# Kernel tuning notes

Measured on AMD Instinct MI355X. Metric: run time of the kernel, lower is better.

## Reference

```python
import jax, jax.numpy as jnp
import numpy as np

N_NODES = 100_000
N_EDGES = 1_600_000
F_DIM = 32


def setup_inputs() -> dict:
    key = jax.random.key(0)
    k1, k2, k3 = jax.random.split(key, 3)
    x = jax.random.normal(k1, (N_NODES, F_DIM), dtype=jnp.float32)
    edge_index = jax.random.randint(k2, (2, N_EDGES), 0, N_NODES, dtype=jnp.int64)
    edge_weight = jax.random.uniform(k3, (N_EDGES,), dtype=jnp.float32)
    w_mp = jnp.array([0.5], dtype=jnp.float32)  # learned scalar parameter
    return {"x": x, "edge_index": edge_index, "edge_weight": edge_weight, "w_mp": w_mp}


def reference(x, edge_index, edge_weight, w_mp):
    # message: ea = w_mp * x[src] * edge_weight  (shape [E, F])
    # aggregate: sum messages into target nodes (aggr='add', source_to_target)
    src = edge_index[0]
    dst = edge_index[1]
    ea = (w_mp * x[src]) * edge_weight[:, None]          # [E, F]
    out = jax.ops.segment_sum(ea, dst, num_segments=x.shape[0])  # [N, F]
    return out
```

## Files before the change

### kernel.cpp

```cpp
#include <hip/hip_runtime.h>


constexpr int N_NODES = 100000;
constexpr int N_EDGES = 1600000;
constexpr int F_DIM   = 32;

constexpr int NPB = 64;
constexpr int NB  = (N_NODES + NPB - 1) / NPB;
constexpr int CAP = 1344;

constexpr int BIN_THREADS = 512;
constexpr int BIN_EPT     = 8;
constexpr int BIN_CHUNK   = BIN_THREADS * BIN_EPT;
constexpr int BIN_BLOCKS  = (N_EDGES + BIN_CHUNK - 1) / BIN_CHUNK;

constexpr int AGG_THREADS = 512;
constexpr int RPT = (CAP + AGG_THREADS - 1) / AGG_THREADS;

constexpr size_t WS_CURSOR  = 0;
constexpr size_t WS_RECORDS = 8192;
constexpr size_t WS_NEEDED  = WS_RECORDS + (size_t)NB * CAP * 8;

__global__ __launch_bounds__(256) void init_cursors(int* __restrict__ gcursor)
{
    int i = blockIdx.x * 256 + threadIdx.x;
    if (i < NB) gcursor[i] = i * CAP;
}

__global__ __launch_bounds__(BIN_THREADS) void bin_edges(
    const int* __restrict__ src, const int* __restrict__ dst,
    const float* __restrict__ ew, const float* __restrict__ w_mp,
    int* __restrict__ gcursor, uint2* __restrict__ records)
{
    __shared__ int lhist[NB];
    __shared__ int lbase[NB];
    for (int i = threadIdx.x; i < NB; i += BIN_THREADS) lhist[i] = 0;
    __syncthreads();

    const float w = w_mp[0];
    const int base_e = blockIdx.x * BIN_CHUNK;
    int   bkt[BIN_EPT];
    uint2 rec[BIN_EPT];

    #pragma unroll
    for (int i = 0; i < BIN_EPT; ++i) {
        int e = base_e + threadIdx.x + i * BIN_THREADS;
        bkt[i] = -1;
        if (e < N_EDGES) {
            int d = dst[e];
            int b = d >> 6;
            bkt[i] = b;
            rec[i].x = __float_as_uint(w * ew[e]);
            rec[i].y = (unsigned)src[e] | ((unsigned)(d & 63) << 24);
            atomicAdd(&lhist[b], 1);
        }
    }
    __syncthreads();

    for (int i = threadIdx.x; i < NB; i += BIN_THREADS) {
        int c = lhist[i];
        lbase[i] = c ? atomicAdd(&gcursor[i], c) : 0;
        lhist[i] = 0;
    }
    __syncthreads();

    #pragma unroll
    for (int i = 0; i < BIN_EPT; ++i) {
        int b = bkt[i];
        if (b >= 0) {
            int pos = lbase[b] + atomicAdd(&lhist[b], 1);
            if (pos < (b + 1) * CAP)
                records[pos] = rec[i];
        }
    }
}

__global__ __launch_bounds__(AGG_THREADS) void sort_gather(
    const int*   __restrict__ gcursor,
    const uint2* __restrict__ records,
    const float* __restrict__ x,
    float*       __restrict__ out)
{
    __shared__ uint2 sorted[CAP];
    __shared__ int   hist[NPB];
    __shared__ int   offs[NPB + 1];
    __shared__ int   cursor[NPB];

    const int b     = blockIdx.x;
    const int t     = threadIdx.x;
    const int rbase = b * CAP;
    const int cnt   = min(gcursor[b] - rbase, CAP);

    if (t < NPB) hist[t] = 0;
    __syncthreads();

    uint2 rec[RPT];
    #pragma unroll
    for (int i = 0; i < RPT; ++i) {
        int j = t + i * AGG_THREADS;
        rec[i].y = 0xFFFFFFFFu;
        if (j < cnt) {
            rec[i] = records[rbase + j];
            atomicAdd(&hist[rec[i].y >> 24], 1);
        }
    }
    __syncthreads();

    if (t < 64) {
        int v   = hist[t];
        int inc = v;
        #pragma unroll
        for (int d = 1; d < 64; d <<= 1) {
            int o = __shfl_up(inc, d, 64);
            if (t >= d) inc += o;
        }
        offs[t + 1] = inc;
        if (t == 0) offs[0] = 0;
        cursor[t] = inc - v;
    }
    __syncthreads();

    #pragma unroll
    for (int i = 0; i < RPT; ++i) {
        if (rec[i].y != 0xFFFFFFFFu) {
            int dl   = rec[i].y >> 24;
            int slot = atomicAdd(&cursor[dl], 1);
            sorted[slot] = rec[i];
        }
    }
    __syncthreads();

    const int node  = t >> 3;
    const int q     = (t & 7) * 4;
    const int gnode = b * NPB + node;
    if (gnode >= N_NODES) return;

    int j  = offs[node];
    int je = offs[node + 1];
    float4 acc = make_float4(0.f, 0.f, 0.f, 0.f);

    for (; j + 4 <= je; j += 4) {
        uint2 r0 = sorted[j + 0];
        uint2 r1 = sorted[j + 1];
        uint2 r2 = sorted[j + 2];
        uint2 r3 = sorted[j + 3];
        const float4 v0 = *reinterpret_cast<const float4*>(
            x + (size_t)(r0.y & 0xFFFFFFu) * F_DIM + q);
        const float4 v1 = *reinterpret_cast<const float4*>(
            x + (size_t)(r1.y & 0xFFFFFFu) * F_DIM + q);
        const float4 v2 = *reinterpret_cast<const float4*>(
            x + (size_t)(r2.y & 0xFFFFFFu) * F_DIM + q);
        const float4 v3 = *reinterpret_cast<const float4*>(
            x + (size_t)(r3.y & 0xFFFFFFu) * F_DIM + q);
        float c0 = __uint_as_float(r0.x), c1 = __uint_as_float(r1.x);
        float c2 = __uint_as_float(r2.x), c3 = __uint_as_float(r3.x);
        acc.x += c0 * v0.x + c1 * v1.x + c2 * v2.x + c3 * v3.x;
        acc.y += c0 * v0.y + c1 * v1.y + c2 * v2.y + c3 * v3.y;
        acc.z += c0 * v0.z + c1 * v1.z + c2 * v2.z + c3 * v3.z;
        acc.w += c0 * v0.w + c1 * v1.w + c2 * v2.w + c3 * v3.w;
    }
    for (; j < je; ++j) {
        uint2 r = sorted[j];
        float c = __uint_as_float(r.x);
        const float4 v = *reinterpret_cast<const float4*>(
            x + (size_t)(r.y & 0xFFFFFFu) * F_DIM + q);
        acc.x += c * v.x;
        acc.y += c * v.y;
        acc.z += c * v.z;
        acc.w += c * v.w;
    }
    *reinterpret_cast<float4*>(out + (size_t)gnode * F_DIM + q) = acc;
}

__global__ __launch_bounds__(256) void gnn_scatter_atomic(
    const float* __restrict__ x, const int* __restrict__ src,
    const int* __restrict__ dst, const float* __restrict__ ew,
    const float* __restrict__ w_mp, float* __restrict__ out)
{
    const float w = w_mp[0];
    int gid = blockIdx.x * blockDim.x + threadIdx.x;
    int e = gid >> 3;
    int qq = (gid & 7) * 4;
    if (e >= N_EDGES) return;
    int s = src[e];
    int d = dst[e];
    float c = w * ew[e];
    const float4 xv = *reinterpret_cast<const float4*>(x + (size_t)s * F_DIM + qq);
    float* op = out + (size_t)d * F_DIM + qq;
    atomicAdd(op + 0, c * xv.x);
    atomicAdd(op + 1, c * xv.y);
    atomicAdd(op + 2, c * xv.z);
    atomicAdd(op + 3, c * xv.w);
}

extern "C" void kernel_launch(void* const* d_in, const int* in_sizes, int n_in,
                              void* d_out, int out_size, void* d_ws, size_t ws_size,
                              hipStream_t stream) {
    const float* x    = (const float*)d_in[0];
    const int*   ei   = (const int*)d_in[1];
    const float* ew   = (const float*)d_in[2];
    const float* w_mp = (const float*)d_in[3];
    float* out = (float*)d_out;

    const int* src = ei;
    const int* dst = ei + N_EDGES;

    if (ws_size < WS_NEEDED) {
        hipMemsetAsync(d_out, 0, (size_t)out_size * sizeof(float), stream);
        int total = N_EDGES * 8;
        gnn_scatter_atomic<<<(total + 255) / 256, 256, 0, stream>>>(
            x, src, dst, ew, w_mp, out);
        return;
    }

    char* ws = (char*)d_ws;
    int*   gcursor = (int*)(ws + WS_CURSOR);
    uint2* records = (uint2*)(ws + WS_RECORDS);

    init_cursors<<<(NB + 255) / 256, 256, 0, stream>>>(gcursor);
    bin_edges<<<BIN_BLOCKS, BIN_THREADS, 0, stream>>>(src, dst, ew, w_mp,
                                                      gcursor, records);
    sort_gather<<<NB, AGG_THREADS, 0, stream>>>(gcursor, records, x, out);
}
```

Baseline: 135.9 us.

## Bin edges into coarse 256-node buckets and accumulate via LDS atomics without sorting

The binning pass now uses 391 coarse buckets of 256 destination nodes instead of 1563 buckets of 64, which cuts the per-block histogram size and the number of global cursor atomics. The aggregation kernel launches four sub-blocks per coarse bucket. Each sub-block scans the whole bucket, ballot-compacts the records for its 64 nodes into LDS, and accumulates into a skewed shared-memory tile with workgroup-scope float atomics, replacing the per-node counting sort. The cost is that every record is read four times, plus LDS atomic contention and non-deterministic summation order.

```diff
diff --git a/kernel.cpp b/kernel.cpp
--- a/kernel.cpp
+++ b/kernel.cpp
@@ -5,26 +5,28 @@
 constexpr int N_EDGES = 1600000;
 constexpr int F_DIM   = 32;
 
-constexpr int NPB = 64;
-constexpr int NB  = (N_NODES + NPB - 1) / NPB;
-constexpr int CAP = 1344;
+constexpr int NPB_C = 256;
+constexpr int NB_C  = (N_NODES + NPB_C - 1) / NPB_C;
+constexpr int CAP_C = 4608;
 
 constexpr int BIN_THREADS = 512;
 constexpr int BIN_EPT     = 8;
 constexpr int BIN_CHUNK   = BIN_THREADS * BIN_EPT;
 constexpr int BIN_BLOCKS  = (N_EDGES + BIN_CHUNK - 1) / BIN_CHUNK;
 
+constexpr int SUBS    = 4;
+constexpr int NPB_F   = NPB_C / SUBS;
+constexpr int MCAP    = 1344;
 constexpr int AGG_THREADS = 512;
-constexpr int RPT = (CAP + AGG_THREADS - 1) / AGG_THREADS;
 
 constexpr size_t WS_CURSOR  = 0;
-constexpr size_t WS_RECORDS = 8192;
-constexpr size_t WS_NEEDED  = WS_RECORDS + (size_t)NB * CAP * 8;
+constexpr size_t WS_RECORDS = 4096;
+constexpr size_t WS_NEEDED  = WS_RECORDS + (size_t)NB_C * CAP_C * 8;
 
 __global__ __launch_bounds__(256) void init_cursors(int* __restrict__ gcursor)
 {
     int i = blockIdx.x * 256 + threadIdx.x;
-    if (i < NB) gcursor[i] = i * CAP;
+    if (i < NB_C) gcursor[i] = i * CAP_C;
 }
 
 __global__ __launch_bounds__(BIN_THREADS) void bin_edges(
@@ -32,9 +34,9 @@
     const float* __restrict__ ew, const float* __restrict__ w_mp,
     int* __restrict__ gcursor, uint2* __restrict__ records)
 {
-    __shared__ int lhist[NB];
-    __shared__ int lbase[NB];
-    for (int i = threadIdx.x; i < NB; i += BIN_THREADS) lhist[i] = 0;
+    __shared__ int lhist[NB_C];
+    __shared__ int lbase[NB_C];
+    if (threadIdx.x < NB_C) lhist[threadIdx.x] = 0;
     __syncthreads();
 
     const float w = w_mp[0];
@@ -48,19 +50,19 @@
         bkt[i] = -1;
         if (e < N_EDGES) {
             int d = dst[e];
-            int b = d >> 6;
+            int b = d >> 8;
             bkt[i] = b;
             rec[i].x = __float_as_uint(w * ew[e]);
-            rec[i].y = (unsigned)src[e] | ((unsigned)(d & 63) << 24);
+            rec[i].y = (unsigned)src[e] | ((unsigned)(d & 255) << 24);
             atomicAdd(&lhist[b], 1);
         }
     }
     __syncthreads();
 
-    for (int i = threadIdx.x; i < NB; i += BIN_THREADS) {
-        int c = lhist[i];
-        lbase[i] = c ? atomicAdd(&gcursor[i], c) : 0;
-        lhist[i] = 0;
+    if (threadIdx.x < NB_C) {
+        int c = lhist[threadIdx.x];
+        lbase[threadIdx.x] = c ? atomicAdd(&gcursor[threadIdx.x], c) : 0;
+        lhist[threadIdx.x] = 0;
     }
     __syncthreads();
 
@@ -69,107 +71,101 @@
         int b = bkt[i];
         if (b >= 0) {
             int pos = lbase[b] + atomicAdd(&lhist[b], 1);
-            if (pos < (b + 1) * CAP)
+            if (pos < (b + 1) * CAP_C)
                 records[pos] = rec[i];
         }
     }
 }
 
-__global__ __launch_bounds__(AGG_THREADS) void sort_gather(
+__device__ __forceinline__ void tile_add(float* tile, int row, int q, int k, float v)
+{
+    __hip_atomic_fetch_add(&tile[(row << 5) + ((q + k + row) & 31)], v,
+                           __ATOMIC_RELAXED, __HIP_MEMORY_SCOPE_WORKGROUP);
+}
+
+__global__ __launch_bounds__(AGG_THREADS) void gather_nosort(
     const int*   __restrict__ gcursor,
     const uint2* __restrict__ records,
     const float* __restrict__ x,
     float*       __restrict__ out)
 {
-    __shared__ uint2 sorted[CAP];
-    __shared__ int   hist[NPB];
-    __shared__ int   offs[NPB + 1];
-    __shared__ int   cursor[NPB];
-
-    const int b     = blockIdx.x;
-    const int t     = threadIdx.x;
-    const int rbase = b * CAP;
-    const int cnt   = min(gcursor[b] - rbase, CAP);
-
-    if (t < NPB) hist[t] = 0;
-    __syncthreads();
-
-    uint2 rec[RPT];
-    #pragma unroll
-    for (int i = 0; i < RPT; ++i) {
-        int j = t + i * AGG_THREADS;
-        rec[i].y = 0xFFFFFFFFu;
-        if (j < cnt) {
-            rec[i] = records[rbase + j];
-            atomicAdd(&hist[rec[i].y >> 24], 1);
+    __shared__ float tile[NPB_F * F_DIM];
+    __shared__ uint2 mine[MCAP];
+    __shared__ int   mcount;
+
+    const int coarse = blockIdx.x >> 2;
+    const unsigned sub = blockIdx.x & 3;
+    const int t = threadIdx.x;
+
+    float4* t4 = reinterpret_cast<float4*>(tile);
+    if (t < NPB_F * F_DIM / 4) t4[t] = make_float4(0.f, 0.f, 0.f, 0.f);
+    if (t == 0) mcount = 0;
+    __syncthreads();
+
+    const int rbase = coarse * CAP_C;
+    const int cnt   = min(gcursor[coarse] - rbase, CAP_C);
+    const int lane  = t & 63;
+    for (int j = t; j < cnt; j += AGG_THREADS) {
+        uint2 r = records[rbase + j];
+        bool match = (r.y >> 30) == sub;
+        unsigned long long m = __ballot(match);
+        if (m) {
+            int lead = __ffsll((unsigned long long)m) - 1;
+            int base = 0;
+            if (lane == lead) base = atomicAdd(&mcount, __popcll(m));
+            base = __shfl(base, lead, 64);
+            if (match) {
+                int slot = base + __popcll(m & ((1ull << lane) - 1));
+                if (slot < MCAP) mine[slot] = r;
+            }
         }
     }
     __syncthreads();
 
-    if (t < 64) {
-        int v   = hist[t];
-        int inc = v;
-        #pragma unroll
-        for (int d = 1; d < 64; d <<= 1) {
-            int o = __shfl_up(inc, d, 64);
-            if (t >= d) inc += o;
-        }
-        offs[t + 1] = inc;
-        if (t == 0) offs[0] = 0;
-        cursor[t] = inc - v;
-    }
-    __syncthreads();
-
-    #pragma unroll
-    for (int i = 0; i < RPT; ++i) {
-        if (rec[i].y != 0xFFFFFFFFu) {
-            int dl   = rec[i].y >> 24;
-            int slot = atomicAdd(&cursor[dl], 1);
-            sorted[slot] = rec[i];
-        }
-    }
-    __syncthreads();
-
-    const int node  = t >> 3;
-    const int q     = (t & 7) * 4;
-    const int gnode = b * NPB + node;
-    if (gnode >= N_NODES) return;
-
-    int j  = offs[node];
-    int je = offs[node + 1];
-    float4 acc = make_float4(0.f, 0.f, 0.f, 0.f);
-
-    for (; j + 4 <= je; j += 4) {
-        uint2 r0 = sorted[j + 0];
-        uint2 r1 = sorted[j + 1];
-        uint2 r2 = sorted[j + 2];
-        uint2 r3 = sorted[j + 3];
+    const int M = min(mcount, MCAP);
+    const int q = (t & 7) * 4;
+    int g = t >> 3;
+    for (; g + 64 < M; g += 128) {
+        uint2 r0 = mine[g];
+        uint2 r1 = mine[g + 64];
         const float4 v0 = *reinterpret_cast<const float4*>(
             x + (size_t)(r0.y & 0xFFFFFFu) * F_DIM + q);
         const float4 v1 = *reinterpret_cast<const float4*>(
             x + (size_t)(r1.y & 0xFFFFFFu) * F_DIM + q);
-        const float4 v2 = *reinterpret_cast<const float4*>(
-            x + (size_t)(r2.y & 0xFFFFFFu) * F_DIM + q);
-        const float4 v3 = *reinterpret_cast<const float4*>(
-            x + (size_t)(r3.y & 0xFFFFFFu) * F_DIM + q);
-        float c0 = __uint_as_float(r0.x), c1 = __uint_as_float(r1.x);
-        float c2 = __uint_as_float(r2.x), c3 = __uint_as_float(r3.x);
-        acc.x += c0 * v0.x + c1 * v1.x + c2 * v2.x + c3 * v3.x;
-        acc.y += c0 * v0.y + c1 * v1.y + c2 * v2.y + c3 * v3.y;
-        acc.z += c0 * v0.z + c1 * v1.z + c2 * v2.z + c3 * v3.z;
-        acc.w += c0 * v0.w + c1 * v1.w + c2 * v2.w + c3 * v3.w;
-    }
-    for (; j < je; ++j) {
-        uint2 r = sorted[j];
-        float c = __uint_as_float(r.x);
+        float c0 = __uint_as_float(r0.x);
+        float c1 = __uint_as_float(r1.x);
+        int row0 = (r0.y >> 24) & 63;
+        int row1 = (r1.y >> 24) & 63;
+        tile_add(tile, row0, q, 0, c0 * v0.x);
+        tile_add(tile, row0, q, 1, c0 * v0.y);
+        tile_add(tile, row0, q, 2, c0 * v0.z);
+        tile_add(tile, row0, q, 3, c0 * v0.w);
+        tile_add(tile, row1, q, 0, c1 * v1.x);
+        tile_add(tile, row1, q, 1, c1 * v1.y);
+        tile_add(tile, row1, q, 2, c1 * v1.z);
+        tile_add(tile, row1, q, 3, c1 * v1.w);
+    }
+    for (; g < M; g += 64) {
+        uint2 r = mine[g];
         const float4 v = *reinterpret_cast<const float4*>(
             x + (size_t)(r.y & 0xFFFFFFu) * F_DIM + q);
-        acc.x += c * v.x;
-        acc.y += c * v.y;
-        acc.z += c * v.z;
-        acc.w += c * v.w;
-    }
-    *reinterpret_cast<float4*>(out + (size_t)gnode * F_DIM + q) = acc;
+        float c = __uint_as_float(r.x);
+        int row = (r.y >> 24) & 63;
+        tile_add(tile, row, q, 0, c * v.x);
+        tile_add(tile, row, q, 1, c * v.y);
+        tile_add(tile, row, q, 2, c * v.z);
+        tile_add(tile, row, q, 3, c * v.w);
+    }
+    __syncthreads();
+
+    const int node0 = coarse * NPB_C + (int)sub * NPB_F;
+    for (int i = t; i < NPB_F * F_DIM; i += AGG_THREADS) {
+        int rr  = i >> 5;
+        int col = i & 31;
+        int n   = node0 + rr;
+        if (n < N_NODES)
+            out[(size_t)n * F_DIM + col] = tile[(rr << 5) + ((col + rr) & 31)];
+    }
 }
 
 __global__ __launch_bounds__(256) void gnn_scatter_atomic(
@@ -217,8 +213,8 @@
     int*   gcursor = (int*)(ws + WS_CURSOR);
     uint2* records = (uint2*)(ws + WS_RECORDS);
 
-    init_cursors<<<(NB + 255) / 256, 256, 0, stream>>>(gcursor);
+    init_cursors<<<(NB_C + 255) / 256, 256, 0, stream>>>(gcursor);
     bin_edges<<<BIN_BLOCKS, BIN_THREADS, 0, stream>>>(src, dst, ew, w_mp,
                                                       gcursor, records);
-    sort_gather<<<NB, AGG_THREADS, 0, stream>>>(gcursor, records, x, out);
-}
+    gather_nosort<<<NB_C * SUBS, AGG_THREADS, 0, stream>>>(gcursor, records, x, out);
+}
```

Result: slower. 400.8 us (+195.0%).

## Bin edges into coarse 256-node buckets and filter sub-buckets in aggregation

Applied to the files above, without the earlier changes.

The binning pass now uses 391 coarse buckets of 256 nodes with 16 edges per thread instead of 1563 buckets of 64 nodes. This shrinks the shared histogram and cuts the number of global cursor atomics per block. Each aggregation block reads the whole coarse bucket and uses ballot-based compaction to keep only the records for its 64-node sub-range, then sorts and gathers as before. The cost is that every coarse bucket's records are read four times in the aggregation stage, and there is an extra compaction pass through shared memory.

```diff
diff --git a/kernel.cpp b/kernel.cpp
--- a/kernel.cpp
+++ b/kernel.cpp
@@ -5,26 +5,29 @@
 constexpr int N_EDGES = 1600000;
 constexpr int F_DIM   = 32;
 
-constexpr int NPB = 64;
-constexpr int NB  = (N_NODES + NPB - 1) / NPB;
-constexpr int CAP = 1344;
+constexpr int NPB_C = 256;
+constexpr int NB_C  = (N_NODES + NPB_C - 1) / NPB_C;
+constexpr int CAP_C = 4608;
 
 constexpr int BIN_THREADS = 512;
-constexpr int BIN_EPT     = 8;
+constexpr int BIN_EPT     = 16;
 constexpr int BIN_CHUNK   = BIN_THREADS * BIN_EPT;
 constexpr int BIN_BLOCKS  = (N_EDGES + BIN_CHUNK - 1) / BIN_CHUNK;
 
+constexpr int SUBS  = 4;
+constexpr int NPB_F = NPB_C / SUBS;
+constexpr int MCAP  = 1344;
 constexpr int AGG_THREADS = 512;
-constexpr int RPT = (CAP + AGG_THREADS - 1) / AGG_THREADS;
+constexpr int RPT = (MCAP + AGG_THREADS - 1) / AGG_THREADS;
 
 constexpr size_t WS_CURSOR  = 0;
-constexpr size_t WS_RECORDS = 8192;
-constexpr size_t WS_NEEDED  = WS_RECORDS + (size_t)NB * CAP * 8;
+constexpr size_t WS_RECORDS = 4096;
+constexpr size_t WS_NEEDED  = WS_RECORDS + (size_t)NB_C * CAP_C * 8;
 
 __global__ __launch_bounds__(256) void init_cursors(int* __restrict__ gcursor)
 {
     int i = blockIdx.x * 256 + threadIdx.x;
-    if (i < NB) gcursor[i] = i * CAP;
+    if (i < NB_C) gcursor[i] = i * CAP_C;
 }
 
 __global__ __launch_bounds__(BIN_THREADS) void bin_edges(
@@ -32,9 +35,9 @@
     const float* __restrict__ ew, const float* __restrict__ w_mp,
     int* __restrict__ gcursor, uint2* __restrict__ records)
 {
-    __shared__ int lhist[NB];
-    __shared__ int lbase[NB];
-    for (int i = threadIdx.x; i < NB; i += BIN_THREADS) lhist[i] = 0;
+    __shared__ int lhist[NB_C];
+    __shared__ int lbase[NB_C];
+    if (threadIdx.x < NB_C) lhist[threadIdx.x] = 0;
     __syncthreads();
 
     const float w = w_mp[0];
@@ -48,19 +51,19 @@
         bkt[i] = -1;
         if (e < N_EDGES) {
             int d = dst[e];
-            int b = d >> 6;
+            int b = d >> 8;
             bkt[i] = b;
             rec[i].x = __float_as_uint(w * ew[e]);
-            rec[i].y = (unsigned)src[e] | ((unsigned)(d & 63) << 24);
+            rec[i].y = (unsigned)src[e] | ((unsigned)(d & 255) << 24);
             atomicAdd(&lhist[b], 1);
         }
     }
     __syncthreads();
 
-    for (int i = threadIdx.x; i < NB; i += BIN_THREADS) {
-        int c = lhist[i];
-        lbase[i] = c ? atomicAdd(&gcursor[i], c) : 0;
-        lhist[i] = 0;
+    if (threadIdx.x < NB_C) {
+        int c = lhist[threadIdx.x];
+        lbase[threadIdx.x] = c ? atomicAdd(&gcursor[threadIdx.x], c) : 0;
+        lhist[threadIdx.x] = 0;
     }
     __syncthreads();
 
@@ -69,7 +72,7 @@
         int b = bkt[i];
         if (b >= 0) {
             int pos = lbase[b] + atomicAdd(&lhist[b], 1);
-            if (pos < (b + 1) * CAP)
+            if (pos < (b + 1) * CAP_C)
                 records[pos] = rec[i];
         }
     }
@@ -81,27 +84,50 @@
     const float* __restrict__ x,
     float*       __restrict__ out)
 {
-    __shared__ uint2 sorted[CAP];
-    __shared__ int   hist[NPB];
-    __shared__ int   offs[NPB + 1];
-    __shared__ int   cursor[NPB];
-
-    const int b     = blockIdx.x;
-    const int t     = threadIdx.x;
-    const int rbase = b * CAP;
-    const int cnt   = min(gcursor[b] - rbase, CAP);
-
-    if (t < NPB) hist[t] = 0;
-    __syncthreads();
-
+    __shared__ uint2 mine[MCAP];
+    __shared__ uint2 sorted[MCAP];
+    __shared__ int   hist[NPB_F];
+    __shared__ int   offs[NPB_F + 1];
+    __shared__ int   cursor[NPB_F];
+    __shared__ int   mcount;
+
+    const int coarse   = blockIdx.x >> 2;
+    const unsigned sub = blockIdx.x & 3;
+    const int t        = threadIdx.x;
+    const int lane     = t & 63;
+
+    if (t < NPB_F) hist[t] = 0;
+    if (t == 0) mcount = 0;
+    __syncthreads();
+
+    const int rbase = coarse * CAP_C;
+    const int cnt   = min(gcursor[coarse] - rbase, CAP_C);
+    for (int j = t; j < cnt; j += AGG_THREADS) {
+        uint2 r = records[rbase + j];
+        bool match = (r.y >> 30) == sub;
+        unsigned long long m = __ballot(match);
+        if (m) {
+            int lead = __ffsll(m) - 1;
+            int base = 0;
+            if (lane == lead) base = atomicAdd(&mcount, __popcll(m));
+            base = __shfl(base, lead, 64);
+            if (match) {
+                int slot = base + __popcll(m & ((1ull << lane) - 1));
+                if (slot < MCAP) mine[slot] = r;
+            }
+        }
+    }
+    __syncthreads();
+
+    const int M = min(mcount, MCAP);
     uint2 rec[RPT];
     #pragma unroll
     for (int i = 0; i < RPT; ++i) {
         int j = t + i * AGG_THREADS;
         rec[i].y = 0xFFFFFFFFu;
-        if (j < cnt) {
-            rec[i] = records[rbase + j];
-            atomicAdd(&hist[rec[i].y >> 24], 1);
+        if (j < M) {
+            rec[i] = mine[j];
+            atomicAdd(&hist[(rec[i].y >> 24) & 63], 1);
         }
     }
     __syncthreads();
@@ -123,8 +149,7 @@
     #pragma unroll
     for (int i = 0; i < RPT; ++i) {
         if (rec[i].y != 0xFFFFFFFFu) {
-            int dl   = rec[i].y >> 24;
-            int slot = atomicAdd(&cursor[dl], 1);
+            int slot = atomicAdd(&cursor[(rec[i].y >> 24) & 63], 1);
             sorted[slot] = rec[i];
         }
     }
@@ -132,7 +157,7 @@
 
     const int node  = t >> 3;
     const int q     = (t & 7) * 4;
-    const int gnode = b * NPB + node;
+    const int gnode = coarse * NPB_C + (int)sub * NPB_F + node;
     if (gnode >= N_NODES) return;
 
     int j  = offs[node];
@@ -217,8 +242,8 @@
     int*   gcursor = (int*)(ws + WS_CURSOR);
     uint2* records = (uint2*)(ws + WS_RECORDS);
 
-    init_cursors<<<(NB + 255) / 256, 256, 0, stream>>>(gcursor);
+    init_cursors<<<(NB_C + 255) / 256, 256, 0, stream>>>(gcursor);
     bin_edges<<<BIN_BLOCKS, BIN_THREADS, 0, stream>>>(src, dst, ew, w_mp,
                                                       gcursor, records);
-    sort_gather<<<NB, AGG_THREADS, 0, stream>>>(gcursor, records, x, out);
-}
+    sort_gather<<<NB_C * SUBS, AGG_THREADS, 0, stream>>>(gcursor, records, x, out);
+}
```

Result: faster. 128.9 us (-5.1%).
